# Performance work log

Hardware: AMD Instinct MI355X
Metric: run time of the kernel (lower is better)

Reference implementation:

```python
import jax, jax.numpy as jnp
import numpy as np

N = 50000      # nodes
E = 800000     # edges (before self-loops)
IN = 64        # in_channels
H = 4          # heads
C = 32         # out_channels per head
HC = H * C     # 128
NEG_SLOPE = 0.2


def setup_inputs() -> dict:
    key = jax.random.key(0)
    ks = jax.random.split(key, 16)
    def p(k, shape):
        return (jax.random.normal(k, shape, jnp.float32) * 0.1)
    x = jax.random.normal(ks[0], (N, IN), jnp.float32)
    edge_index = jax.random.randint(ks[1], (2, E), 0, N, dtype=jnp.int32)
    return {
        "x": x,
        "Wl1": p(ks[2], (IN, HC)),  "bl1": p(ks[3], (HC,)),
        "Wr1": p(ks[4], (IN, HC)),  "br1": p(ks[5], (HC,)),
        "att1": p(ks[6], (H, C)),   "bias1": p(ks[7], (HC,)),
        "Wl2": p(ks[8], (HC, HC)),  "bl2": p(ks[9], (HC,)),
        "Wr2": p(ks[10], (HC, HC)), "br2": p(ks[11], (HC,)),
        "att2": p(ks[12], (H, C)),  "bias2": p(ks[13], (HC,)),
        "edge_index": edge_index,
    }


def gatv2_layer(x, src, dst, Wl, bl, Wr, br, att, bias):
    """GATv2Conv (concat=True, eval mode). src/dst include self-loops."""
    n = x.shape[0]
    h, c = att.shape
    xl = (x @ Wl + bl).reshape(n, h, c)   # source-side transform
    xr = (x @ Wr + br).reshape(n, h, c)   # target-side transform
    # per-edge GATv2 score: att . LeakyReLU(x_j + x_i)
    e = jax.nn.leaky_relu(xl[src] + xr[dst], NEG_SLOPE)   # [E', H, C]
    score = jnp.einsum('ehc,hc->eh', e, att)              # [E', H]
    # segment softmax over destination node
    m = jax.ops.segment_max(score, dst, num_segments=n)   # [N, H]
    ex = jnp.exp(score - m[dst])
    denom = jax.ops.segment_sum(ex, dst, num_segments=n)  # [N, H]
    alpha = ex / denom[dst]                               # [E', H]
    # weighted scatter-aggregate of source messages
    out = jax.ops.segment_sum(alpha[:, :, None] * xl[src], dst, num_segments=n)
    return out.reshape(n, h * c) + bias


def reference(x, Wl1, bl1, Wr1, br1, att1, bias1,
              Wl2, bl2, Wr2, br2, att2, bias2, edge_index):
    n = x.shape[0]
    loops = jnp.arange(n, dtype=edge_index.dtype)
    src = jnp.concatenate([edge_index[0], loops])  # PyG add_self_loops=True
    dst = jnp.concatenate([edge_index[1], loops])
    h = jax.nn.relu(gatv2_layer(x, src, dst, Wl1, bl1, Wr1, br1, att1, bias1))
    out = jax.nn.relu(gatv2_layer(h, src, dst, Wl2, bl2, Wr2, br2, att2, bias2))
    return out
```

## Files before the change

### kernel.cpp

```cpp
#include <hip/hip_runtime.h>

#define LEAKY 0.2f
#define NBSHIFT 8
#define TILE 4096

typedef __attribute__((ext_vector_type(8))) short  bfrag;
typedef __attribute__((ext_vector_type(4))) float  f32x4;

__device__ __forceinline__ unsigned bf16rne(float v) {
    unsigned u = __float_as_uint(v);
    return (u + 0x7FFF + ((u >> 16) & 1)) >> 16;
}
__device__ __forceinline__ float bf16tof(unsigned b) { return __uint_as_float(b << 16); }

#define DPPADD(p, ctrl)                                                       \
    p += __int_as_float(__builtin_amdgcn_mov_dpp(__float_as_int(p), ctrl,     \
                                                 0xF, 0xF, true))
__device__ __forceinline__ float rowsum16(float p) {
    DPPADD(p, 0xB1);
    DPPADD(p, 0x4E);
    DPPADD(p, 0x124);
    DPPADD(p, 0x128);
    return p;
}


__global__ __launch_bounds__(256) void bucket_hist(const int* __restrict__ dst,
                                                   int* __restrict__ bcnt, int E, int nb) {
    __shared__ int h[256];
    h[threadIdx.x] = 0;
    __syncthreads();
    for (int e = blockIdx.x * 256 + threadIdx.x; e < E; e += gridDim.x * 256)
        atomicAdd(&h[dst[e] >> NBSHIFT], 1);
    __syncthreads();
    int v = h[threadIdx.x];
    if (threadIdx.x < nb && v) atomicAdd(&bcnt[threadIdx.x], v);
}

__global__ __launch_bounds__(256) void bucket_scan(const int* __restrict__ bcnt,
                                                   int* __restrict__ bbase,
                                                   int* __restrict__ gwoff,
                                                   int* __restrict__ rowptr,
                                                   int E, int nb, int n) {
    __shared__ int s[256];
    const int t = threadIdx.x;
    int v = (t < nb) ? bcnt[t] : 0;
    s[t] = v;
    __syncthreads();
    for (int off = 1; off < 256; off <<= 1) {
        int a = (t >= off) ? s[t - off] : 0;
        __syncthreads();
        s[t] += a;
        __syncthreads();
    }
    int excl = s[t] - v;
    if (t < nb) { bbase[t] = excl; gwoff[t] = excl; }
    if (t == 0) { bbase[nb] = E; rowptr[n] = E; }
}

__global__ __launch_bounds__(256) void multisplit(const int* __restrict__ src,
                                                  const int* __restrict__ dst,
                                                  int* __restrict__ gwoff,
                                                  int2* __restrict__ pairs, int E, int nb) {
    __shared__ int hist[256], lofs[256], gb[256];
    __shared__ int2 st[TILE];
    const int t = threadIdx.x;
    const int tile0 = blockIdx.x * TILE;
    const int tend = min(tile0 + TILE, E);
    hist[t] = 0;
    __syncthreads();
    for (int e = tile0 + t; e < tend; e += 256)
        atomicAdd(&hist[dst[e] >> NBSHIFT], 1);
    __syncthreads();
    int v = hist[t];
    lofs[t] = v;
    __syncthreads();
    for (int off = 1; off < 256; off <<= 1) {
        int a = (t >= off) ? lofs[t - off] : 0;
        __syncthreads();
        lofs[t] += a;
        __syncthreads();
    }
    int excl = lofs[t] - v;
    __syncthreads();
    lofs[t] = excl;
    if (t < nb && v > 0) gb[t] = atomicAdd(&gwoff[t], v);
    hist[t] = 0;
    __syncthreads();
    for (int e = tile0 + t; e < tend; e += 256) {
        int d = dst[e];
        int b = d >> NBSHIFT;
        int r = atomicAdd(&hist[b], 1);
        st[lofs[b] + r] = make_int2(src[e], d);
    }
    __syncthreads();
    const int total = tend - tile0;
    for (int i = t; i < total; i += 256) {
        int2 p = st[i];
        int b = p.y >> NBSHIFT;
        pairs[gb[b] + (i - lofs[b])] = p;
    }
}

__global__ __launch_bounds__(256) void bucket_sort(const int2* __restrict__ pairs,
                                                   const int* __restrict__ bbase,
                                                   int* __restrict__ rowptr,
                                                   int* __restrict__ ssrc, int n) {
    __shared__ int hist[256], ofs[256];
    const int b = blockIdx.x, t = threadIdx.x;
    const int base = b << NBSHIFT;
    const int pbeg = bbase[b], pend = bbase[b + 1];
    hist[t] = 0;
    __syncthreads();
    for (int i = pbeg + t; i < pend; i += 256)
        atomicAdd(&hist[pairs[i].y - base], 1);
    __syncthreads();
    int v = hist[t];
    ofs[t] = v;
    __syncthreads();
    for (int off = 1; off < 256; off <<= 1) {
        int a = (t >= off) ? ofs[t - off] : 0;
        __syncthreads();
        ofs[t] += a;
        __syncthreads();
    }
    int excl = ofs[t] - v;
    __syncthreads();
    ofs[t] = excl;
    const int node = base + t;
    if (node < n) rowptr[node] = pbeg + excl;
    __syncthreads();
    for (int i = pbeg + t; i < pend; i += 256) {
        int2 p = pairs[i];
        int pos = atomicAdd(&ofs[p.y - base], 1);
        ssrc[pbeg + pos] = p.x;
    }
}


__global__ void split_x(const float* __restrict__ x, ushort* __restrict__ xhi,
                        ushort* __restrict__ xlo, int total4) {
    int i = blockIdx.x * blockDim.x + threadIdx.x;
    if (i >= total4) return;
    float4 v = reinterpret_cast<const float4*>(x)[i];
    ushort4 h, l;
    float* vp = &v.x;
    ushort* hp = &h.x;
    ushort* lp = &l.x;
#pragma unroll
    for (int j = 0; j < 4; ++j) {
        unsigned hb = bf16rne(vp[j]);
        hp[j] = (ushort)hb;
        lp[j] = (ushort)bf16rne(vp[j] - bf16tof(hb));
    }
    reinterpret_cast<ushort4*>(xhi)[i] = h;
    reinterpret_cast<ushort4*>(xlo)[i] = l;
}


__global__ void pack_W(const float* __restrict__ Wl, const float* __restrict__ Wr,
                       ushort* __restrict__ Bhi, ushort* __restrict__ Blo, int K) {
    int tid = blockIdx.x * blockDim.x + threadIdx.x;
    if (tid >= K * 256) return;
    int k = tid >> 8;
    int c = tid & 255;
    float w = (c < 128) ? Wl[k * 128 + c] : Wr[k * 128 + (c - 128)];
    int s = k >> 5, kin = k & 31, kgrp = kin >> 3, j = kin & 7;
    int f = c >> 4, cin = c & 15;
    int lane = kgrp * 16 + cin;
    size_t pos = ((size_t)(s * 16 + f) * 64 + lane) * 8 + j;
    unsigned hb = bf16rne(w);
    Bhi[pos] = (ushort)hb;
    Blo[pos] = (ushort)bf16rne(w - bf16tof(hb));
}


template<int K>
__global__ __launch_bounds__(256) void gemm_mfma(
    const ushort* __restrict__ Ahi, const ushort* __restrict__ Alo,
    const ushort* __restrict__ Bhi, const ushort* __restrict__ Blo,
    const float* __restrict__ bl, const float* __restrict__ br,
    ushort* __restrict__ xlb, float* __restrict__ xr, int n)
{
    __shared__ ushort BshH[2 * 8 * 64 * 8];
    __shared__ ushort BshL[2 * 8 * 64 * 8];
    const int t = threadIdx.x;
    const int w = t >> 6;
    const int lane = t & 63;
    const int half = blockIdx.y;
    const int r0 = blockIdx.x * 64 + w * 16;
    const int rl = lane & 15;
    const int kg = lane >> 4;
    int arow = r0 + rl; if (arow >= n) arow = 0;

    const float4* __restrict__ gH = reinterpret_cast<const float4*>(Bhi);
    const float4* __restrict__ gL = reinterpret_cast<const float4*>(Blo);
    float4* __restrict__ sH = reinterpret_cast<float4*>(BshH);
    float4* __restrict__ sL = reinterpret_cast<float4*>(BshL);

    f32x4 acc[8];
#pragma unroll
    for (int f = 0; f < 8; ++f) acc[f] = (f32x4){0.f, 0.f, 0.f, 0.f};

#pragma unroll
    for (int sg = 0; sg < K / 64; ++sg) {
        if (sg) __syncthreads();
#pragma unroll
        for (int i = t; i < 1024; i += 256) {
            int ss = i >> 9, fl = (i >> 6) & 7, ln = i & 63;
            int gidx = ((2 * sg + ss) * 16 + half * 8 + fl) * 64 + ln;
            sH[i] = gH[gidx];
            sL[i] = gL[gidx];
        }
        __syncthreads();

#pragma unroll
        for (int ss = 0; ss < 2; ++ss) {
            const int s = 2 * sg + ss;
            const size_t ao = (size_t)arow * K + s * 32 + kg * 8;
            bfrag ahi = *reinterpret_cast<const bfrag*>(&Ahi[ao]);
            bfrag alo = *reinterpret_cast<const bfrag*>(&Alo[ao]);
#pragma unroll
            for (int fl = 0; fl < 8; ++fl) {
                const int lofs = ((ss * 8 + fl) * 64 + lane) * 8;
                bfrag bhi = *reinterpret_cast<const bfrag*>(&BshH[lofs]);
                bfrag blo = *reinterpret_cast<const bfrag*>(&BshL[lofs]);
                acc[fl] = __builtin_amdgcn_mfma_f32_16x16x32_bf16(alo, bhi, acc[fl], 0, 0, 0);
                acc[fl] = __builtin_amdgcn_mfma_f32_16x16x32_bf16(ahi, blo, acc[fl], 0, 0, 0);
                acc[fl] = __builtin_amdgcn_mfma_f32_16x16x32_bf16(ahi, bhi, acc[fl], 0, 0, 0);
            }
        }
    }

    const int cin = lane & 15;
    const float* __restrict__ bias_ = half ? br : bl;
#pragma unroll
    for (int fl = 0; fl < 8; ++fl) {
        const int cc = fl * 16 + cin;
        const float bv = bias_[cc];
#pragma unroll
        for (int j = 0; j < 4; ++j) {
            const int rr = r0 + kg * 4 + j;
            if (rr < n) {
                const float v = acc[fl][j] + bv;
                if (half) xr[(size_t)rr * 128 + cc] = v;
                else      xlb[(size_t)rr * 128 + cc] = (ushort)bf16rne(v);
            }
        }
    }
}


template<int OUTMODE>
__global__ __launch_bounds__(256) void gat_agg(
    const ushort* __restrict__ xlb, const float* __restrict__ xr,
    const float* __restrict__ att, const float* __restrict__ bias,
    const int* __restrict__ rowptr, const int* __restrict__ ssrc,
    float* __restrict__ out, ushort* __restrict__ ohi, ushort* __restrict__ olo,
    int n)
{
    const int node = blockIdx.x * 4 + (threadIdx.x >> 6);
    if (node >= n) return;
    const int lane = threadIdx.x & 63;

    const uint* __restrict__ xlu = reinterpret_cast<const uint*>(xlb);
    const float2 a2  = *reinterpret_cast<const float2*>(&att[lane * 2]);
    const float2 xrv = *reinterpret_cast<const float2*>(&xr[(size_t)node * 128 + lane * 2]);

    float den = 0.f, acc0 = 0.f, acc1 = 0.f;

#define EDGE(u)                                                       \
    {                                                                 \
        const float x0 = __uint_as_float((u) << 16);                  \
        const float x1 = __uint_as_float((u) & 0xFFFF0000u);          \
        float e0 = x0 + xrv.x, e1 = x1 + xrv.y;                       \
        e0 = e0 > 0.f ? e0 : LEAKY * e0;                              \
        e1 = e1 > 0.f ? e1 : LEAKY * e1;                              \
        float p = rowsum16(e0 * a2.x + e1 * a2.y);                    \
        float ex = __expf(p);                                         \
        den  += ex;                                                   \
        acc0 += ex * x0;                                              \
        acc1 += ex * x1;                                              \
    }

    {
        uint u = xlu[(size_t)node * 64 + lane];
        EDGE(u);
    }

    int i = rowptr[node];
    const int end = rowptr[node + 1];
    for (; i + 8 <= end; i += 8) {
        int s0 = ssrc[i],     s1 = ssrc[i + 1], s2 = ssrc[i + 2], s3 = ssrc[i + 3];
        int s4 = ssrc[i + 4], s5 = ssrc[i + 5], s6 = ssrc[i + 6], s7 = ssrc[i + 7];
        uint u0 = xlu[(size_t)s0 * 64 + lane];
        uint u1 = xlu[(size_t)s1 * 64 + lane];
        uint u2 = xlu[(size_t)s2 * 64 + lane];
        uint u3 = xlu[(size_t)s3 * 64 + lane];
        uint u4 = xlu[(size_t)s4 * 64 + lane];
        uint u5 = xlu[(size_t)s5 * 64 + lane];
        uint u6 = xlu[(size_t)s6 * 64 + lane];
        uint u7 = xlu[(size_t)s7 * 64 + lane];
        EDGE(u0); EDGE(u1); EDGE(u2); EDGE(u3);
        EDGE(u4); EDGE(u5); EDGE(u6); EDGE(u7);
    }
    for (; i < end; ++i) {
        uint u = xlu[(size_t)ssrc[i] * 64 + lane];
        EDGE(u);
    }
#undef EDGE

    const float rden = 1.f / den;
    float o0 = fmaxf(acc0 * rden + bias[lane * 2],     0.f);
    float o1 = fmaxf(acc1 * rden + bias[lane * 2 + 1], 0.f);

    if (OUTMODE == 0) {
        *reinterpret_cast<float2*>(&out[(size_t)node * 128 + lane * 2]) =
            make_float2(o0, o1);
    } else {
        unsigned h0 = bf16rne(o0), h1 = bf16rne(o1);
        ushort2 hv = make_ushort2((ushort)h0, (ushort)h1);
        ushort2 lv = make_ushort2((ushort)bf16rne(o0 - bf16tof(h0)),
                                  (ushort)bf16rne(o1 - bf16tof(h1)));
        *reinterpret_cast<ushort2*>(&ohi[(size_t)node * 128 + lane * 2]) = hv;
        *reinterpret_cast<ushort2*>(&olo[(size_t)node * 128 + lane * 2]) = lv;
    }
}


extern "C" void kernel_launch(void* const* d_in, const int* in_sizes, int n_in,
                              void* d_out, int out_size, void* d_ws, size_t ws_size,
                              hipStream_t stream)
{
    const float* x     = (const float*)d_in[0];
    const float* Wl1   = (const float*)d_in[1];
    const float* bl1   = (const float*)d_in[2];
    const float* Wr1   = (const float*)d_in[3];
    const float* br1   = (const float*)d_in[4];
    const float* att1  = (const float*)d_in[5];
    const float* bias1 = (const float*)d_in[6];
    const float* Wl2   = (const float*)d_in[7];
    const float* bl2   = (const float*)d_in[8];
    const float* Wr2   = (const float*)d_in[9];
    const float* br2   = (const float*)d_in[10];
    const float* att2  = (const float*)d_in[11];
    const float* bias2 = (const float*)d_in[12];
    const int*   eidx  = (const int*)d_in[13];

    const int n = in_sizes[0] / 64;
    const int E = in_sizes[13] / 2;
    const int* src = eidx;
    const int* dst = eidx + E;
    const int nb = (n + 255) >> 8;

    char* ws = (char*)d_ws;
    size_t off = 0;
    auto alloc = [&](size_t bytes) -> void* {
        void* p = ws + off;
        off = (off + bytes + 255) & ~(size_t)255;
        return p;
    };
    int* rowptr   = (int*)alloc((size_t)(n + 1) * 4);
    int* ssrc     = (int*)alloc((size_t)E * 4);
    int* bcnt     = (int*)alloc((size_t)nb * 4);
    int* bbase    = (int*)alloc((size_t)(nb + 1) * 4);
    int* gwoff    = (int*)alloc((size_t)nb * 4);
    ushort* B1hi  = (ushort*)alloc((size_t)64  * 256 * 2);
    ushort* B1lo  = (ushort*)alloc((size_t)64  * 256 * 2);
    ushort* B2hi  = (ushort*)alloc((size_t)128 * 256 * 2);
    ushort* B2lo  = (ushort*)alloc((size_t)128 * 256 * 2);
    ushort* xreg  = (ushort*)alloc((size_t)n * 128 * 2 * 2);
    ushort* xhi1  = xreg;
    ushort* xlo1  = xreg + (size_t)n * 64;
    ushort* hhi   = xreg;
    ushort* hlo   = xreg + (size_t)n * 128;
    ushort* xlb   = (ushort*)alloc((size_t)n * 128 * 2);
    float* xrbuf  = (float*)alloc((size_t)n * 128 * 4);
    int2* pairs   = (int2*)xlb;
    float* outp   = (float*)d_out;

    hipMemsetAsync(bcnt, 0, (size_t)nb * 4, stream);
    bucket_hist<<<128, 256, 0, stream>>>(dst, bcnt, E, nb);
    bucket_scan<<<1, 256, 0, stream>>>(bcnt, bbase, gwoff, rowptr, E, nb, n);
    multisplit<<<(E + TILE - 1) / TILE, 256, 0, stream>>>(src, dst, gwoff, pairs, E, nb);
    bucket_sort<<<nb, 256, 0, stream>>>(pairs, bbase, rowptr, ssrc, n);

    const int total4 = n * 64 / 4;
    split_x<<<(total4 + 255) / 256, 256, 0, stream>>>(x, xhi1, xlo1, total4);
    pack_W<<<(64  * 256 + 255) / 256, 256, 0, stream>>>(Wl1, Wr1, B1hi, B1lo, 64);
    pack_W<<<(128 * 256 + 255) / 256, 256, 0, stream>>>(Wl2, Wr2, B2hi, B2lo, 128);

    const dim3 ggrid((n + 63) / 64, 2);

    gemm_mfma<64><<<ggrid, 256, 0, stream>>>(xhi1, xlo1, B1hi, B1lo, bl1, br1,
                                             xlb, xrbuf, n);
    gat_agg<1><<<(n + 3) / 4, 256, 0, stream>>>(xlb, xrbuf, att1, bias1, rowptr, ssrc,
                                                nullptr, hhi, hlo, n);

    gemm_mfma<128><<<ggrid, 256, 0, stream>>>(hhi, hlo, B2hi, B2lo, bl2, br2,
                                              xlb, xrbuf, n);
    gat_agg<0><<<(n + 3) / 4, 256, 0, stream>>>(xlb, xrbuf, att2, bias2, rowptr, ssrc,
                                                outp, nullptr, nullptr, n);
}
```

Baseline: 210.0 us.

## Process two edges per wavefront in GAT aggregation using half-wave split

The aggregation kernel now has each half of the 64-lane wavefront handle a different source edge. Each lane loads 4 bf16 features (8 bytes) instead of 2, so per-head reduction needs only an 8-lane DPP sum. The two halves' partial softmax denominators and accumulators are combined with a cross-half shuffle at the end. This doubles the edges processed per instruction and widens gather loads, at the cost of masking for odd edge counts and an extra final reduction.

```diff
diff --git a/kernel.cpp b/kernel.cpp
--- a/kernel.cpp
+++ b/kernel.cpp
@@ -16,11 +16,10 @@
 #define DPPADD(p, ctrl)                                                       \
     p += __int_as_float(__builtin_amdgcn_mov_dpp(__float_as_int(p), ctrl,     \
                                                  0xF, 0xF, true))
-__device__ __forceinline__ float rowsum16(float p) {
+__device__ __forceinline__ float rowsum8(float p) {
     DPPADD(p, 0xB1);
     DPPADD(p, 0x4E);
-    DPPADD(p, 0x124);
-    DPPADD(p, 0x128);
+    DPPADD(p, 0x141);
     return p;
 }
 
@@ -262,68 +261,102 @@
     const int node = blockIdx.x * 4 + (threadIdx.x >> 6);
     if (node >= n) return;
     const int lane = threadIdx.x & 63;
-
-    const uint* __restrict__ xlu = reinterpret_cast<const uint*>(xlb);
-    const float2 a2  = *reinterpret_cast<const float2*>(&att[lane * 2]);
-    const float2 xrv = *reinterpret_cast<const float2*>(&xr[(size_t)node * 128 + lane * 2]);
-
-    float den = 0.f, acc0 = 0.f, acc1 = 0.f;
-
-#define EDGE(u)                                                       \
+    const int m = lane & 31;
+    const bool hiHalf = lane >= 32;
+
+    const uint2* __restrict__ xlu = reinterpret_cast<const uint2*>(xlb);
+    const float4 a4  = reinterpret_cast<const float4*>(att)[m];
+    const float4 xrv = reinterpret_cast<const float4*>(xr)[(size_t)node * 32 + m];
+
+    float den = 0.f;
+    float4 acc = make_float4(0.f, 0.f, 0.f, 0.f);
+
+#define GATHER(sA, sB) xlu[(size_t)(hiHalf ? (sB) : (sA)) * 32 + m]
+#define PAIR(u, MSK)                                                  \
     {                                                                 \
-        const float x0 = __uint_as_float((u) << 16);                  \
-        const float x1 = __uint_as_float((u) & 0xFFFF0000u);          \
+        const float x0 = __uint_as_float((u).x << 16);                \
+        const float x1 = __uint_as_float((u).x & 0xFFFF0000u);        \
+        const float x2 = __uint_as_float((u).y << 16);                \
+        const float x3 = __uint_as_float((u).y & 0xFFFF0000u);        \
         float e0 = x0 + xrv.x, e1 = x1 + xrv.y;                       \
+        float e2 = x2 + xrv.z, e3 = x3 + xrv.w;                       \
         e0 = e0 > 0.f ? e0 : LEAKY * e0;                              \
         e1 = e1 > 0.f ? e1 : LEAKY * e1;                              \
-        float p = rowsum16(e0 * a2.x + e1 * a2.y);                    \
-        float ex = __expf(p);                                         \
-        den  += ex;                                                   \
-        acc0 += ex * x0;                                              \
-        acc1 += ex * x1;                                              \
-    }
-
-    {
-        uint u = xlu[(size_t)node * 64 + lane];
-        EDGE(u);
+        e2 = e2 > 0.f ? e2 : LEAKY * e2;                              \
+        e3 = e3 > 0.f ? e3 : LEAKY * e3;                              \
+        float p = e0 * a4.x + e1 * a4.y + e2 * a4.z + e3 * a4.w;      \
+        p = rowsum8(p);                                               \
+        float ex = __expf(p) MSK;                                     \
+        den += ex;                                                    \
+        acc.x += ex * x0; acc.y += ex * x1;                           \
+        acc.z += ex * x2; acc.w += ex * x3;                           \
     }
 
     int i = rowptr[node];
     const int end = rowptr[node + 1];
+
+    {
+        const bool vB = i < end;
+        const int sB = vB ? ssrc[i] : node;
+        uint2 u = GATHER(node, sB);
+        const float msk = (hiHalf && !vB) ? 0.f : 1.f;
+        PAIR(u, * msk);
+        if (vB) ++i;
+    }
+
     for (; i + 8 <= end; i += 8) {
         int s0 = ssrc[i],     s1 = ssrc[i + 1], s2 = ssrc[i + 2], s3 = ssrc[i + 3];
         int s4 = ssrc[i + 4], s5 = ssrc[i + 5], s6 = ssrc[i + 6], s7 = ssrc[i + 7];
-        uint u0 = xlu[(size_t)s0 * 64 + lane];
-        uint u1 = xlu[(size_t)s1 * 64 + lane];
-        uint u2 = xlu[(size_t)s2 * 64 + lane];
-        uint u3 = xlu[(size_t)s3 * 64 + lane];
-        uint u4 = xlu[(size_t)s4 * 64 + lane];
-        uint u5 = xlu[(size_t)s5 * 64 + lane];
-        uint u6 = xlu[(size_t)s6 * 64 + lane];
-        uint u7 = xlu[(size_t)s7 * 64 + lane];
-        EDGE(u0); EDGE(u1); EDGE(u2); EDGE(u3);
-        EDGE(u4); EDGE(u5); EDGE(u6); EDGE(u7);
-    }
-    for (; i < end; ++i) {
-        uint u = xlu[(size_t)ssrc[i] * 64 + lane];
-        EDGE(u);
-    }
-#undef EDGE
-
-    const float rden = 1.f / den;
-    float o0 = fmaxf(acc0 * rden + bias[lane * 2],     0.f);
-    float o1 = fmaxf(acc1 * rden + bias[lane * 2 + 1], 0.f);
-
-    if (OUTMODE == 0) {
-        *reinterpret_cast<float2*>(&out[(size_t)node * 128 + lane * 2]) =
-            make_float2(o0, o1);
-    } else {
-        unsigned h0 = bf16rne(o0), h1 = bf16rne(o1);
-        ushort2 hv = make_ushort2((ushort)h0, (ushort)h1);
-        ushort2 lv = make_ushort2((ushort)bf16rne(o0 - bf16tof(h0)),
-                                  (ushort)bf16rne(o1 - bf16tof(h1)));
-        *reinterpret_cast<ushort2*>(&ohi[(size_t)node * 128 + lane * 2]) = hv;
-        *reinterpret_cast<ushort2*>(&olo[(size_t)node * 128 + lane * 2]) = lv;
+        uint2 u0 = GATHER(s0, s1);
+        uint2 u1 = GATHER(s2, s3);
+        uint2 u2 = GATHER(s4, s5);
+        uint2 u3 = GATHER(s6, s7);
+        PAIR(u0, );
+        PAIR(u1, );
+        PAIR(u2, );
+        PAIR(u3, );
+    }
+    for (; i + 2 <= end; i += 2) {
+        int s0 = ssrc[i], s1 = ssrc[i + 1];
+        uint2 u = GATHER(s0, s1);
+        PAIR(u, );
+    }
+    if (i < end) {
+        int s0 = ssrc[i];
+        uint2 u = GATHER(s0, s0);
+        const float msk = hiHalf ? 0.f : 1.f;
+        PAIR(u, * msk);
+    }
+#undef PAIR
+#undef GATHER
+
+    den   += __shfl_xor(den,   32);
+    acc.x += __shfl_xor(acc.x, 32);
+    acc.y += __shfl_xor(acc.y, 32);
+    acc.z += __shfl_xor(acc.z, 32);
+    acc.w += __shfl_xor(acc.w, 32);
+
+    if (!hiHalf) {
+        const float4 b4 = reinterpret_cast<const float4*>(bias)[m];
+        const float r = 1.f / den;
+        const float o0 = fmaxf(acc.x * r + b4.x, 0.f);
+        const float o1 = fmaxf(acc.y * r + b4.y, 0.f);
+        const float o2 = fmaxf(acc.z * r + b4.z, 0.f);
+        const float o3 = fmaxf(acc.w * r + b4.w, 0.f);
+        if (OUTMODE == 0) {
+            reinterpret_cast<float4*>(out)[(size_t)node * 32 + m] =
+                make_float4(o0, o1, o2, o3);
+        } else {
+            unsigned h0 = bf16rne(o0), h1 = bf16rne(o1);
+            unsigned h2 = bf16rne(o2), h3 = bf16rne(o3);
+            ushort4 hv = make_ushort4((ushort)h0, (ushort)h1, (ushort)h2, (ushort)h3);
+            ushort4 lv = make_ushort4((ushort)bf16rne(o0 - bf16tof(h0)),
+                                      (ushort)bf16rne(o1 - bf16tof(h1)),
+                                      (ushort)bf16rne(o2 - bf16tof(h2)),
+                                      (ushort)bf16rne(o3 - bf16tof(h3)));
+            reinterpret_cast<ushort4*>(ohi)[(size_t)node * 32 + m] = hv;
+            reinterpret_cast<ushort4*>(olo)[(size_t)node * 32 + m] = lv;
+        }
     }
 }
 
```

Result: faster. 202.6 us (-3.5%).

## Store source features head-major and process one head per block with four edges per wavefront

Applied to the files above, without the earlier changes.

The GEMM now writes the bf16 source-side features in a head-major layout ([head][node][32]). The aggregation kernel launches separate blocks per head, and each wavefront handles four edges at once, one per 16-lane slot, with masked tail handling and a cross-slot shuffle reduction at the end. The aim is a smaller per-head working set of gathered rows, which should improve cache locality and give more memory-level parallelism per wave. In exchange the grid is four times larger, the target-side row and index loads are repeated for every head, and the masked padding lanes do wasted work.

```diff
diff --git a/kernel.cpp b/kernel.cpp
--- a/kernel.cpp
+++ b/kernel.cpp
@@ -244,7 +244,8 @@
             if (rr < n) {
                 const float v = acc[fl][j] + bv;
                 if (half) xr[(size_t)rr * 128 + cc] = v;
-                else      xlb[(size_t)rr * 128 + cc] = (ushort)bf16rne(v);
+                else      xlb[((size_t)(cc >> 5) * n + rr) * 32 + (cc & 31)] =
+                              (ushort)bf16rne(v);
             }
         }
     }
@@ -253,77 +254,91 @@
 
 template<int OUTMODE>
 __global__ __launch_bounds__(256) void gat_agg(
-    const ushort* __restrict__ xlb, const float* __restrict__ xr,
+    const ushort* __restrict__ xlb,
+    const float* __restrict__ xr,
     const float* __restrict__ att, const float* __restrict__ bias,
     const int* __restrict__ rowptr, const int* __restrict__ ssrc,
     float* __restrict__ out, ushort* __restrict__ ohi, ushort* __restrict__ olo,
-    int n)
+    int n, int nodeblks)
 {
-    const int node = blockIdx.x * 4 + (threadIdx.x >> 6);
+    const int head = blockIdx.x / nodeblks;
+    const int nblk = blockIdx.x - head * nodeblks;
+    const int node = nblk * 4 + (threadIdx.x >> 6);
     if (node >= n) return;
     const int lane = threadIdx.x & 63;
-
-    const uint* __restrict__ xlu = reinterpret_cast<const uint*>(xlb);
-    const float2 a2  = *reinterpret_cast<const float2*>(&att[lane * 2]);
-    const float2 xrv = *reinterpret_cast<const float2*>(&xr[(size_t)node * 128 + lane * 2]);
-
-    float den = 0.f, acc0 = 0.f, acc1 = 0.f;
-
-#define EDGE(u)                                                       \
+    const int slot = lane >> 4;
+    const int m = lane & 15;
+
+    const uint* __restrict__ xlu =
+        reinterpret_cast<const uint*>(xlb) + (size_t)head * n * 16;
+    const float2 a2  = *reinterpret_cast<const float2*>(&att[head * 32 + m * 2]);
+    const float2 xrv = *reinterpret_cast<const float2*>(
+        &xr[(size_t)node * 128 + head * 32 + m * 2]);
+
+    float den = 0.f;
+    float2 acc = make_float2(0.f, 0.f);
+
+#define PAIR(s, MSK)                                                  \
     {                                                                 \
-        const float x0 = __uint_as_float((u) << 16);                  \
-        const float x1 = __uint_as_float((u) & 0xFFFF0000u);          \
+        const uint u = xlu[(size_t)(s) * 16 + m];                     \
+        const float x0 = __uint_as_float(u << 16);                    \
+        const float x1 = __uint_as_float(u & 0xFFFF0000u);            \
         float e0 = x0 + xrv.x, e1 = x1 + xrv.y;                       \
         e0 = e0 > 0.f ? e0 : LEAKY * e0;                              \
         e1 = e1 > 0.f ? e1 : LEAKY * e1;                              \
         float p = rowsum16(e0 * a2.x + e1 * a2.y);                    \
-        float ex = __expf(p);                                         \
-        den  += ex;                                                   \
-        acc0 += ex * x0;                                              \
-        acc1 += ex * x1;                                              \
-    }
-
-    {
-        uint u = xlu[(size_t)node * 64 + lane];
-        EDGE(u);
+        float ex = __expf(p) MSK;                                     \
+        den += ex;                                                    \
+        acc.x += ex * x0;                                             \
+        acc.y += ex * x1;                                             \
     }
 
     int i = rowptr[node];
     const int end = rowptr[node + 1];
-    for (; i + 8 <= end; i += 8) {
-        int s0 = ssrc[i],     s1 = ssrc[i + 1], s2 = ssrc[i + 2], s3 = ssrc[i + 3];
-        int s4 = ssrc[i + 4], s5 = ssrc[i + 5], s6 = ssrc[i + 6], s7 = ssrc[i + 7];
-        uint u0 = xlu[(size_t)s0 * 64 + lane];
-        uint u1 = xlu[(size_t)s1 * 64 + lane];
-        uint u2 = xlu[(size_t)s2 * 64 + lane];
-        uint u3 = xlu[(size_t)s3 * 64 + lane];
-        uint u4 = xlu[(size_t)s4 * 64 + lane];
-        uint u5 = xlu[(size_t)s5 * 64 + lane];
-        uint u6 = xlu[(size_t)s6 * 64 + lane];
-        uint u7 = xlu[(size_t)s7 * 64 + lane];
-        EDGE(u0); EDGE(u1); EDGE(u2); EDGE(u3);
-        EDGE(u4); EDGE(u5); EDGE(u6); EDGE(u7);
-    }
-    for (; i < end; ++i) {
-        uint u = xlu[(size_t)ssrc[i] * 64 + lane];
-        EDGE(u);
-    }
-#undef EDGE
-
-    const float rden = 1.f / den;
-    float o0 = fmaxf(acc0 * rden + bias[lane * 2],     0.f);
-    float o1 = fmaxf(acc1 * rden + bias[lane * 2 + 1], 0.f);
-
-    if (OUTMODE == 0) {
-        *reinterpret_cast<float2*>(&out[(size_t)node * 128 + lane * 2]) =
-            make_float2(o0, o1);
-    } else {
-        unsigned h0 = bf16rne(o0), h1 = bf16rne(o1);
-        ushort2 hv = make_ushort2((ushort)h0, (ushort)h1);
-        ushort2 lv = make_ushort2((ushort)bf16rne(o0 - bf16tof(h0)),
-                                  (ushort)bf16rne(o1 - bf16tof(h1)));
-        *reinterpret_cast<ushort2*>(&ohi[(size_t)node * 128 + lane * 2]) = hv;
-        *reinterpret_cast<ushort2*>(&olo[(size_t)node * 128 + lane * 2]) = lv;
+
+    {
+        const int nv = min(end - i, 3);
+        const int s = (slot == 0) ? node
+                                  : ((slot <= nv) ? ssrc[i + slot - 1] : node);
+        const float msk = (slot <= nv) ? 1.f : 0.f;
+        PAIR(s, * msk);
+        i += nv;
+    }
+
+    for (; i + 4 <= end; i += 4) {
+        const int s = ssrc[i + slot];
+        PAIR(s, );
+    }
+    {
+        const int rem = end - i;
+        if (rem > 0) {
+            const int s = (slot < rem) ? ssrc[i + slot] : node;
+            const float msk = (slot < rem) ? 1.f : 0.f;
+            PAIR(s, * msk);
+        }
+    }
+#undef PAIR
+
+    den   += __shfl_xor(den,   16); den   += __shfl_xor(den,   32);
+    acc.x += __shfl_xor(acc.x, 16); acc.x += __shfl_xor(acc.x, 32);
+    acc.y += __shfl_xor(acc.y, 16); acc.y += __shfl_xor(acc.y, 32);
+
+    if (lane < 16) {
+        const float2 b2 = *reinterpret_cast<const float2*>(&bias[head * 32 + m * 2]);
+        const float r = 1.f / den;
+        const float o0 = fmaxf(acc.x * r + b2.x, 0.f);
+        const float o1 = fmaxf(acc.y * r + b2.y, 0.f);
+        const size_t oidx = (size_t)node * 128 + head * 32 + m * 2;
+        if (OUTMODE == 0) {
+            *reinterpret_cast<float2*>(&out[oidx]) = make_float2(o0, o1);
+        } else {
+            unsigned h0 = bf16rne(o0), h1 = bf16rne(o1);
+            *reinterpret_cast<ushort2*>(&ohi[oidx]) =
+                make_ushort2((ushort)h0, (ushort)h1);
+            *reinterpret_cast<ushort2*>(&olo[oidx]) =
+                make_ushort2((ushort)bf16rne(o0 - bf16tof(h0)),
+                             (ushort)bf16rne(o1 - bf16tof(h1)));
+        }
     }
 }
 
@@ -391,14 +406,16 @@
     pack_W<<<(128 * 256 + 255) / 256, 256, 0, stream>>>(Wl2, Wr2, B2hi, B2lo, 128);
 
     const dim3 ggrid((n + 63) / 64, 2);
+    const int nodeblks = (n + 3) / 4;
+    const int agrid = nodeblks * 4;
 
     gemm_mfma<64><<<ggrid, 256, 0, stream>>>(xhi1, xlo1, B1hi, B1lo, bl1, br1,
                                              xlb, xrbuf, n);
-    gat_agg<1><<<(n + 3) / 4, 256, 0, stream>>>(xlb, xrbuf, att1, bias1, rowptr, ssrc,
-                                                nullptr, hhi, hlo, n);
+    gat_agg<1><<<agrid, 256, 0, stream>>>(xlb, xrbuf, att1, bias1, rowptr, ssrc,
+                                          nullptr, hhi, hlo, n, nodeblks);
 
     gemm_mfma<128><<<ggrid, 256, 0, stream>>>(hhi, hlo, B2hi, B2lo, bl2, br2,
                                               xlb, xrbuf, n);
-    gat_agg<0><<<(n + 3) / 4, 256, 0, stream>>>(xlb, xrbuf, att2, bias2, rowptr, ssrc,
-                                                outp, nullptr, nullptr, n);
-}
+    gat_agg<0><<<agrid, 256, 0, stream>>>(xlb, xrbuf, att2, bias2, rowptr, ssrc,
+                                          outp, nullptr, nullptr, n, nodeblks);
+}
```

Result: slower. 341.2 us (+62.5%).
